# Optimization experiments

Measured on AMD Instinct MI355X. Metric: run time of the kernel, lower is better.

## Reference

```python
import jax, jax.numpy as jnp
import numpy as np

B, T, DIM, H = 2048, 16, 512, 8
INNER = 4 * DIM  # GEGLU inner dim
NUM_REL = 2 * T - 1


def _ln(x, g, b, eps=1e-5):
    m = jnp.mean(x, -1, keepdims=True)
    v = jnp.var(x, -1, keepdims=True)
    return (x - m) * jax.lax.rsqrt(v + eps) * g + b


def _temporal_attn(x, mask, g, b, wq, wk, wv, wo, bo, pe):
    # x: (B, T, C); mask: (1, T, T) bool; pe: (2T-1, C)
    Bn, Tn, C = x.shape
    d = C // H
    scale = d ** -0.5
    res = x
    xn = _ln(x, g, b)
    q = (xn @ wq).reshape(Bn, Tn, H, d).transpose(0, 2, 1, 3)  # (B,H,T,d)
    k = (xn @ wk).reshape(Bn, Tn, H, d).transpose(0, 2, 1, 3)
    v = (xn @ wv).reshape(Bn, Tn, H, d).transpose(0, 2, 1, 3)
    sim = jnp.einsum('bhmd,bhnd->bhmn', q, k)
    # contextual(2) relative position bias: project rel-pos embeddings through to_q/to_k
    rel = jnp.arange(Tn)[None, :] - jnp.arange(Tn)[:, None] + (Tn - 1)  # (T,T) in [0, 2T-2]
    P = pe[rel]                              # (T, T, C)
    Kr = (P @ wk).reshape(Tn, Tn, H, d)      # (T, T, H, d)
    Qr = (P @ wq).reshape(Tn, Tn, H, d)
    bias = jnp.einsum('bhmd,mnhd->bhmn', q, Kr) + jnp.einsum('bhnd,mnhd->bhmn', k, Qr)
    sim = (sim + bias) * scale
    sim = jnp.where(mask[:, None], sim, -jnp.finfo(sim.dtype).max)
    attn = jax.nn.softmax(sim, axis=-1)
    out = jnp.einsum('bhmn,bhnd->bhmd', attn, v)
    out = out.transpose(0, 2, 1, 3).reshape(Bn, Tn, C)
    return out @ wo + bo + res


def _geglu_ff(x, g, b, w1, b1, w2, b2):
    xn = _ln(x, g, b)
    h = xn @ w1 + b1                         # (B, T, 2*INNER)
    a, gate = jnp.split(h, 2, axis=-1)
    y = a * jax.nn.gelu(gate, approximate=False)
    return y @ w2 + b2 + x


def setup_inputs() -> dict:
    key = jax.random.key(0)
    ks = jax.random.split(key, 24)
    s = 0.02
    d = {
        'x': jax.random.normal(ks[0], (B, T, DIM), jnp.float32),
        'femb': jax.random.normal(ks[1], (T, DIM), jnp.float32),
        'attn_mask': jnp.ones((1, T, T), dtype=bool),
    }
    for i, base in [(2, '1'), (10, '2')]:
        d['n%s_g' % base] = jnp.ones((DIM,), jnp.float32)
        d['n%s_b' % base] = jnp.zeros((DIM,), jnp.float32)
        d['wq%s' % base] = jax.random.normal(ks[i], (DIM, DIM), jnp.float32) * s
        d['wk%s' % base] = jax.random.normal(ks[i + 1], (DIM, DIM), jnp.float32) * s
        d['wv%s' % base] = jax.random.normal(ks[i + 2], (DIM, DIM), jnp.float32) * s
        d['wo%s' % base] = jax.random.normal(ks[i + 3], (DIM, DIM), jnp.float32) * s
        d['bo%s' % base] = jnp.zeros((DIM,), jnp.float32)
        d['pe%s' % base] = jax.random.normal(ks[i + 4], (NUM_REL, DIM), jnp.float32) * s
    d['n3_g'] = jnp.ones((DIM,), jnp.float32)
    d['n3_b'] = jnp.zeros((DIM,), jnp.float32)
    d['ffw1'] = jax.random.normal(ks[20], (DIM, 2 * INNER), jnp.float32) * s
    d['ffb1'] = jnp.zeros((2 * INNER,), jnp.float32)
    d['ffw2'] = jax.random.normal(ks[21], (INNER, DIM), jnp.float32) * s
    d['ffb2'] = jnp.zeros((DIM,), jnp.float32)
    return d


def reference(x, femb,
              n1_g, n1_b, wq1, wk1, wv1, wo1, bo1, pe1,
              n2_g, n2_b, wq2, wk2, wv2, wo2, bo2, pe2,
              n3_g, n3_b, ffw1, ffb1, ffw2, ffb2,
              attn_mask):
    # femb is accepted but unused, matching TemporalTransformerBlock._forward
    x = _temporal_attn(x, attn_mask, n1_g, n1_b, wq1, wk1, wv1, wo1, bo1, pe1)
    x = _temporal_attn(x, attn_mask, n2_g, n2_b, wq2, wk2, wv2, wo2, bo2, pe2)
    x = _geglu_ff(x, n3_g, n3_b, ffw1, ffb1, ffw2, ffb2)
    return x
```

## Files before the change

### kernel.cpp

```cpp
#include <hip/hip_runtime.h>

typedef unsigned int uint;
typedef unsigned short ushort;

typedef float f32x4 __attribute__((ext_vector_type(4)));
typedef short bf16x8 __attribute__((ext_vector_type(8)));

using gas1 = const uint __attribute__((address_space(1)))*;
using las3 = uint __attribute__((address_space(3)))*;

static constexpr int TB    = 2048;
static constexpr int TT    = 16;
static constexpr int TD    = 512;
static constexpr int TH    = 8;
static constexpr int HD    = 64;
static constexpr int NROWS = TB * TT;
static constexpr int NREL  = 2 * TT - 1;
static constexpr int INNER = 2048;

__device__ __forceinline__ float bf2f(uint h) {
    union { uint u; float f; } x; x.u = h << 16; return x.f;
}
__device__ __forceinline__ ushort f2bf(float f) {
    union { float f; uint u; } x; x.f = f;
    uint r = x.u + 0x7fffu + ((x.u >> 16) & 1u);
    return (ushort)(r >> 16);
}
__device__ __forceinline__ void unpack8(uint4 v, float* f) {
    f[0] = bf2f(v.x & 0xffffu); f[1] = bf2f(v.x >> 16);
    f[2] = bf2f(v.y & 0xffffu); f[3] = bf2f(v.y >> 16);
    f[4] = bf2f(v.z & 0xffffu); f[5] = bf2f(v.z >> 16);
    f[6] = bf2f(v.w & 0xffffu); f[7] = bf2f(v.w >> 16);
}
__device__ __forceinline__ uint pck(float a, float b) {
    return (uint)f2bf(a) | ((uint)f2bf(b) << 16);
}
__device__ __forceinline__ uint4 pack8(const float* f) {
    return make_uint4(pck(f[0], f[1]), pck(f[2], f[3]), pck(f[4], f[5]), pck(f[6], f[7]));
}
__device__ __forceinline__ bool is_f32(const uint* probe) { return probe[0] == 0x3F800000u; }
__device__ __forceinline__ float ldraw(const void* p, size_t i, bool f32) {
    return f32 ? ((const float*)p)[i] : bf2f(((const ushort*)p)[i]);
}

struct TrP { const void* in[8]; ushort* out[8]; };
__global__ __launch_bounds__(256)
void tr8_k(TrP p, const uint* __restrict__ probe) {
    const bool f32 = is_f32(probe);
    const void* in  = p.in[blockIdx.z];
    ushort*     out = p.out[blockIdx.z];
    __shared__ ushort t[32][33];
    const int bx = blockIdx.x, by = blockIdx.y;
    const int x = threadIdx.x, y = threadIdx.y;
    #pragma unroll
    for (int i = 0; i < 4; ++i) {
        const size_t src = (size_t)(by * 32 + y + i * 8) * TD + bx * 32 + x;
        t[y + i * 8][x] = f32 ? f2bf(((const float*)in)[src]) : ((const ushort*)in)[src];
    }
    __syncthreads();
    #pragma unroll
    for (int i = 0; i < 4; ++i)
        out[(size_t)(bx * 32 + y + i * 8) * TD + by * 32 + x] = t[x][y + i * 8];
}

__global__ __launch_bounds__(256)
void transpose_k(const void* __restrict__ in, ushort* __restrict__ out, int R, int C,
                 const uint* __restrict__ probe) {
    const bool f32 = is_f32(probe);
    __shared__ ushort t[32][33];
    const int bx = blockIdx.x, by = blockIdx.y;
    const int x = threadIdx.x, y = threadIdx.y;
    #pragma unroll
    for (int i = 0; i < 4; ++i) {
        const size_t src = (size_t)(by * 32 + y + i * 8) * C + bx * 32 + x;
        t[y + i * 8][x] = f32 ? f2bf(((const float*)in)[src]) : ((const ushort*)in)[src];
    }
    __syncthreads();
    #pragma unroll
    for (int i = 0; i < 4; ++i)
        out[(size_t)(bx * 32 + y + i * 8) * R + by * 32 + x] = t[x][y + i * 8];
}

struct PewP { const void* pe[4]; const void* w[4]; ushort* out[4]; };
__global__ __launch_bounds__(256)
void pew4_k(PewP p, const uint* __restrict__ probe) {
    const bool f32 = is_f32(probe);
    const int z = blockIdx.z;
    const void* pe = p.pe[z];
    const void* w  = p.w[z];
    ushort*    out = p.out[z];
    const int c = blockIdx.x * 256 + threadIdx.x;
    const int r = blockIdx.y;
    float acc = 0.f;
    for (int k = 0; k < TD; ++k)
        acc += ldraw(pe, (size_t)r * TD + k, f32) * ldraw(w, (size_t)k * TD + c, f32);
    out[r * TD + c] = f2bf(acc);
}

template<bool RAW>
__global__ __launch_bounds__(256)
void ln_k(const void* __restrict__ xin, const void* __restrict__ gw,
          const void* __restrict__ bw, ushort* __restrict__ out,
          const uint* __restrict__ probe) {
    const bool f32 = is_f32(probe);
    const int row = blockIdx.x * 4 + (threadIdx.x >> 6);
    const int l = threadIdx.x & 63;
    const int c0 = l * 8;
    float v[8];
    if (RAW && f32) {
        const float* x = (const float*)xin + (size_t)row * TD + c0;
        const float4 a = *(const float4*)x;
        const float4 b = *(const float4*)(x + 4);
        v[0] = a.x; v[1] = a.y; v[2] = a.z; v[3] = a.w;
        v[4] = b.x; v[5] = b.y; v[6] = b.z; v[7] = b.w;
    } else {
        unpack8(*(const uint4*)((const ushort*)xin + (size_t)row * TD + c0), v);
    }
    float s = 0.f, s2 = 0.f;
    #pragma unroll
    for (int j = 0; j < 8; ++j) { s += v[j]; s2 += v[j] * v[j]; }
    #pragma unroll
    for (int off = 32; off; off >>= 1) {
        s  += __shfl_xor(s, off);
        s2 += __shfl_xor(s2, off);
    }
    const float mean = s * (1.f / TD);
    const float var  = s2 * (1.f / TD) - mean * mean;
    const float rstd = rsqrtf(var + 1e-5f);
    float gf[8], bf[8], r[8];
    if (f32) {
        const float* g = (const float*)gw + c0;
        const float* b = (const float*)bw + c0;
        #pragma unroll
        for (int j = 0; j < 8; ++j) { gf[j] = g[j]; bf[j] = b[j]; }
    } else {
        unpack8(*(const uint4*)((const ushort*)gw + c0), gf);
        unpack8(*(const uint4*)((const ushort*)bw + c0), bf);
    }
    #pragma unroll
    for (int j = 0; j < 8; ++j) r[j] = (v[j] - mean) * rstd * gf[j] + bf[j];
    *(uint4*)(out + (size_t)row * TD + c0) = pack8(r);
}

template<bool GEGLU>
__global__ __launch_bounds__(256)
void gemm_bt(const ushort* __restrict__ A, const ushort* __restrict__ Bt,
             const void* __restrict__ bias, const void* Res, void* C,
             int M, int N, int K, int resraw, int outraw, int outrow0,
             const uint* __restrict__ probe) {
    const bool f32 = is_f32(probe);
    constexpr int BN = GEGLU ? 64 : 128;
    constexpr int NI = GEGLU ? 2 : 4;
    __shared__ ushort sA[2][128 * 32];
    __shared__ ushort sB[2][BN * 32];
    __shared__ ushort sB2[GEGLU ? 2 : 1][GEGLU ? BN * 32 : 16];

    const int tid = threadIdx.x;

    const int lin = blockIdx.y * gridDim.x + blockIdx.x;
    const int cgx = gridDim.x >> 3;
    const int xcd = lin & 7;
    const int idx = lin >> 3;
    const int bx  = xcd * cgx + (idx % cgx);
    const int by  = idx / cgx;

    const int m0 = bx * 128;
    const int n0 = by * BN;
    const int w  = tid >> 6;
    const int l  = tid & 63;
    const int wm = (w >> 1) * 64;
    const int wn = (w & 1) * (BN / 2);
    const int fr = l & 15;
    const int fg = l >> 4;

    const int srow = tid >> 2;
    const int spart = (tid & 3) * 8;
    const ushort* gA0 = A  + (size_t)(m0 + srow) * K + spart;
    const ushort* gA1 = gA0 + (size_t)64 * K;
    const ushort* gB0 = Bt + (size_t)(n0 + srow) * K + spart;
    const ushort* gB1 = gB0 + (size_t)64 * K;
    const ushort* gG0 = Bt + (size_t)(N + n0 + srow) * K + spart;

    f32x4 acc[4][NI]  = {};
    f32x4 acc2[4][NI] = {};

    const int NT = K >> 5;

    auto stage = [&](int t, int buf) {
        const int kt = t * 32;
        __builtin_amdgcn_global_load_lds((gas1)(const void*)(gA0 + kt),
            (las3)(void*)(&sA[buf][tid * 8]), 16, 0, 0);
        __builtin_amdgcn_global_load_lds((gas1)(const void*)(gA1 + kt),
            (las3)(void*)(&sA[buf][(tid + 256) * 8]), 16, 0, 0);
        __builtin_amdgcn_global_load_lds((gas1)(const void*)(gB0 + kt),
            (las3)(void*)(&sB[buf][tid * 8]), 16, 0, 0);
        if constexpr (!GEGLU)
            __builtin_amdgcn_global_load_lds((gas1)(const void*)(gB1 + kt),
                (las3)(void*)(&sB[buf][(tid + 256) * 8]), 16, 0, 0);
        if constexpr (GEGLU)
            __builtin_amdgcn_global_load_lds((gas1)(const void*)(gG0 + kt),
                (las3)(void*)(&sB2[buf][tid * 8]), 16, 0, 0);
    };

    stage(0, 0);
    __syncthreads();

    for (int t = 0; t < NT; ++t) {
        const int cur = t & 1;
        if (t + 1 < NT) stage(t + 1, cur ^ 1);

        bf16x8 af[4], bn[NI], bg[NI];
        #pragma unroll
        for (int i = 0; i < 4; ++i)
            af[i] = *(const bf16x8*)&sA[cur][(wm + i * 16 + fr) * 32 + fg * 8];
        #pragma unroll
        for (int i = 0; i < NI; ++i) {
            bn[i] = *(const bf16x8*)&sB[cur][(wn + i * 16 + fr) * 32 + fg * 8];
            if constexpr (GEGLU)
                bg[i] = *(const bf16x8*)&sB2[cur][(wn + i * 16 + fr) * 32 + fg * 8];
        }
        #pragma unroll
        for (int mi = 0; mi < 4; ++mi)
            #pragma unroll
            for (int ni = 0; ni < NI; ++ni) {
                acc[mi][ni] = __builtin_amdgcn_mfma_f32_16x16x32_bf16(af[mi], bn[ni], acc[mi][ni], 0, 0, 0);
                if constexpr (GEGLU)
                    acc2[mi][ni] = __builtin_amdgcn_mfma_f32_16x16x32_bf16(af[mi], bg[ni], acc2[mi][ni], 0, 0, 0);
            }
        __syncthreads();
    }

    #pragma unroll
    for (int mi = 0; mi < 4; ++mi)
        #pragma unroll
        for (int ni = 0; ni < NI; ++ni) {
            const int col = n0 + wn + ni * 16 + fr;
            const float bv = bias ? ldraw(bias, col, f32) : 0.f;
            float bgv = 0.f;
            if constexpr (GEGLU) bgv = bias ? ldraw(bias, (size_t)N + col, f32) : 0.f;
            #pragma unroll
            for (int j = 0; j < 4; ++j) {
                const int row = m0 + wm + mi * 16 + fg * 4 + j;
                const size_t idx2 = (size_t)(outrow0 + row) * N + col;
                float v = acc[mi][ni][j] + bv;
                if constexpr (GEGLU) {
                    const float gt = acc2[mi][ni][j] + bgv;
                    v = v * (0.5f * gt * (1.f + erff(gt * 0.70710678118654752f)));
                }
                if (Res) v += resraw ? ldraw(Res, idx2, f32) : bf2f(((const ushort*)Res)[idx2]);
                if (outraw && f32) ((float*)C)[idx2] = v;
                else               ((ushort*)C)[idx2] = f2bf(v);
            }
        }
}

__global__ __launch_bounds__(64)
void attn_k(const ushort* __restrict__ qkv, const ushort* __restrict__ peWk,
            const ushort* __restrict__ peWq, ushort* __restrict__ out) {
    __shared__ ushort sQ[16][72], sK[16][72], sV[16][72];
    __shared__ ushort sPk[31][72], sPq[31][72];
    __shared__ float sP[16][20];

    const int tid = threadIdx.x;
    const int b = blockIdx.x >> 3;
    const int h = blockIdx.x & 7;
    const size_t rowbase = (size_t)b * 16 * (3 * TD) + h * HD;

    #pragma unroll
    for (int it = 0; it < 2; ++it) {
        const int c = tid + it * 64;
        const int m = c >> 3, part = c & 7;
        const ushort* src = qkv + rowbase + (size_t)m * (3 * TD) + part * 8;
        *(uint4*)&sQ[m][part * 8] = *(const uint4*)(src);
        *(uint4*)&sK[m][part * 8] = *(const uint4*)(src + TD);
        *(uint4*)&sV[m][part * 8] = *(const uint4*)(src + 2 * TD);
    }
    #pragma unroll
    for (int it = 0; it < 4; ++it) {
        const int c = tid + it * 64;
        if (c < NREL * 8) {
            const int r = c >> 3, part = c & 7;
            *(uint4*)&sPk[r][part * 8] = *(const uint4*)&peWk[(size_t)r * TD + h * HD + part * 8];
            *(uint4*)&sPq[r][part * 8] = *(const uint4*)&peWq[(size_t)r * TD + h * HD + part * 8];
        }
    }
    __syncthreads();

    const int m = tid & 15;
    const int g = tid >> 4;

    float aqk[4] = {0, 0, 0, 0}, ab1[4] = {0, 0, 0, 0}, ab2[4] = {0, 0, 0, 0};
    for (int dc = 0; dc < 8; ++dc) {
        float qf[8];
        unpack8(*(const uint4*)&sQ[m][dc * 8], qf);
        #pragma unroll
        for (int t = 0; t < 4; ++t) {
            const int n = g * 4 + t;
            const int rel = n - m + (TT - 1);
            float kf[8], pk[8], pq[8];
            unpack8(*(const uint4*)&sK[n][dc * 8], kf);
            unpack8(*(const uint4*)&sPk[rel][dc * 8], pk);
            unpack8(*(const uint4*)&sPq[rel][dc * 8], pq);
            #pragma unroll
            for (int j = 0; j < 8; ++j) {
                aqk[t] += qf[j] * kf[j];
                ab1[t] += qf[j] * pk[j];
                ab2[t] += kf[j] * pq[j];
            }
        }
    }
    float sim[4];
    #pragma unroll
    for (int t = 0; t < 4; ++t) sim[t] = (aqk[t] + ab1[t] + ab2[t]) * 0.125f;

    float mx = fmaxf(fmaxf(sim[0], sim[1]), fmaxf(sim[2], sim[3]));
    mx = fmaxf(mx, __shfl_xor(mx, 16));
    mx = fmaxf(mx, __shfl_xor(mx, 32));
    float e[4], ssum = 0.f;
    #pragma unroll
    for (int t = 0; t < 4; ++t) { e[t] = __expf(sim[t] - mx); ssum += e[t]; }
    ssum += __shfl_xor(ssum, 16);
    ssum += __shfl_xor(ssum, 32);
    const float inv = 1.f / ssum;
    #pragma unroll
    for (int t = 0; t < 4; ++t) sP[m][g * 4 + t] = e[t] * inv;
    __syncthreads();

    float o[16] = {};
    for (int n = 0; n < 16; ++n) {
        const float pv = sP[m][n];
        float vf[16];
        unpack8(*(const uint4*)&sV[n][g * 16], vf);
        unpack8(*(const uint4*)&sV[n][g * 16 + 8], vf + 8);
        #pragma unroll
        for (int i = 0; i < 16; ++i) o[i] += pv * vf[i];
    }
    ushort* dst = out + (size_t)(b * 16 + m) * TD + h * HD + g * 16;
    *(uint4*)dst = pack8(o);
    *(uint4*)(dst + 8) = pack8(o + 8);
}

extern "C" void kernel_launch(void* const* d_in, const int* in_sizes, int n_in,
                              void* d_out, int out_size, void* d_ws, size_t ws_size,
                              hipStream_t stream) {
    (void)in_sizes; (void)n_in; (void)out_size;

    const void* X   = d_in[0];
    const void* n1g = d_in[3];
    const void* n1b = d_in[4];
    const void* wq1 = d_in[5];
    const void* wk1 = d_in[6];
    const void* wv1 = d_in[7];
    const void* wo1 = d_in[8];
    const void* bo1 = d_in[9];
    const void* pe1 = d_in[10];
    const void* n2g = d_in[11];
    const void* n2b = d_in[12];
    const void* wq2 = d_in[13];
    const void* wk2 = d_in[14];
    const void* wv2 = d_in[15];
    const void* wo2 = d_in[16];
    const void* bo2 = d_in[17];
    const void* pe2 = d_in[18];
    const void* n3g = d_in[19];
    const void* n3b = d_in[20];
    const void* fw1 = d_in[21];
    const void* fb1 = d_in[22];
    const void* fw2 = d_in[23];
    const void* fb2 = d_in[24];
    const uint* probe = (const uint*)n1g;

    ushort* ws    = (ushort*)d_ws;
    ushort* xn    = ws;
    ushort* qkv   = xn + (size_t)NROWS * TD;
    ushort* x12   = qkv + (size_t)NROWS * (3 * TD);
    ushort* p     = x12 + (size_t)NROWS * TD;
    ushort* qkvT1 = p; p += (size_t)3 * TD * TD;
    ushort* woT1  = p; p += (size_t)TD * TD;
    ushort* qkvT2 = p; p += (size_t)3 * TD * TD;
    ushort* woT2  = p; p += (size_t)TD * TD;
    ushort* w1T   = p; p += (size_t)2 * INNER * TD;
    ushort* w2T   = p; p += (size_t)TD * INNER;
    ushort* peWk1 = p; p += NREL * TD;
    ushort* peWq1 = p; p += NREL * TD;
    ushort* peWk2 = p; p += NREL * TD;
    ushort* peWq2 = p; p += NREL * TD;
    const size_t need_bytes = (size_t)(p - ws) * sizeof(ushort);
    if (ws_size < need_bytes) return;

    ushort* aout = xn;
    ushort* ybuf = qkv;

    const dim3 tpb(32, 8);
    TrP trp;
    trp.in[0] = wq1; trp.out[0] = qkvT1;
    trp.in[1] = wk1; trp.out[1] = qkvT1 + TD * TD;
    trp.in[2] = wv1; trp.out[2] = qkvT1 + 2 * TD * TD;
    trp.in[3] = wo1; trp.out[3] = woT1;
    trp.in[4] = wq2; trp.out[4] = qkvT2;
    trp.in[5] = wk2; trp.out[5] = qkvT2 + TD * TD;
    trp.in[6] = wv2; trp.out[6] = qkvT2 + 2 * TD * TD;
    trp.in[7] = wo2; trp.out[7] = woT2;
    tr8_k<<<dim3(TD / 32, TD / 32, 8), tpb, 0, stream>>>(trp, probe);
    transpose_k<<<dim3(2 * INNER / 32, TD / 32), tpb, 0, stream>>>(fw1, w1T, TD, 2 * INNER, probe);
    transpose_k<<<dim3(TD / 32, INNER / 32), tpb, 0, stream>>>(fw2, w2T, INNER, TD, probe);
    PewP pwp;
    pwp.pe[0] = pe1; pwp.w[0] = wk1; pwp.out[0] = peWk1;
    pwp.pe[1] = pe1; pwp.w[1] = wq1; pwp.out[1] = peWq1;
    pwp.pe[2] = pe2; pwp.w[2] = wk2; pwp.out[2] = peWk2;
    pwp.pe[3] = pe2; pwp.w[3] = wq2; pwp.out[3] = peWq2;
    pew4_k<<<dim3(2, NREL, 4), 256, 0, stream>>>(pwp, probe);

    const int gm = NROWS / 128;

    ln_k<true><<<NROWS / 4, 256, 0, stream>>>(X, n1g, n1b, xn, probe);
    gemm_bt<false><<<dim3(gm, 12), 256, 0, stream>>>(
        xn, qkvT1, nullptr, nullptr, qkv, NROWS, 3 * TD, TD, 0, 0, 0, probe);
    attn_k<<<TB * TH, 64, 0, stream>>>(qkv, peWk1, peWq1, aout);
    gemm_bt<false><<<dim3(gm, 4), 256, 0, stream>>>(
        aout, woT1, bo1, X, x12, NROWS, TD, TD, 1, 0, 0, probe);

    ln_k<false><<<NROWS / 4, 256, 0, stream>>>(x12, n2g, n2b, xn, probe);
    gemm_bt<false><<<dim3(gm, 12), 256, 0, stream>>>(
        xn, qkvT2, nullptr, nullptr, qkv, NROWS, 3 * TD, TD, 0, 0, 0, probe);
    attn_k<<<TB * TH, 64, 0, stream>>>(qkv, peWk2, peWq2, aout);
    gemm_bt<false><<<dim3(gm, 4), 256, 0, stream>>>(
        aout, woT2, bo2, x12, x12, NROWS, TD, TD, 0, 0, 0, probe);

    ln_k<false><<<NROWS / 4, 256, 0, stream>>>(x12, n3g, n3b, xn, probe);
    const int chunk = NROWS / 2;
    for (int hh = 0; hh < 2; ++hh) {
        gemm_bt<true><<<dim3(chunk / 128, INNER / 64), 256, 0, stream>>>(
            xn + (size_t)hh * chunk * TD, w1T, fb1, nullptr, ybuf,
            chunk, INNER, TD, 0, 0, 0, probe);
        gemm_bt<false><<<dim3(chunk / 128, TD / 128), 256, 0, stream>>>(
            ybuf, w2T, fb2, (const void*)x12, d_out,
            chunk, TD, INNER, 0, 1, hh * chunk, probe);
    }
}
```

Before: 975.1 us.

## Triple-buffer GEMM LDS stages with partial vmcnt waits and XOR-swizzled layout

Moves the bf16 GEMM main loop from double to triple buffering so two k-tiles are in flight. Each iteration waits only until the oldest stage's loads have landed (s_waitcnt vmcnt) instead of a full __syncthreads. It also XOR-swizzles the 16-byte chunk position within each 32-element LDS row, on both the global source column and the fragment read offset, to cut bank conflicts on the MFMA fragment loads. This costs 50% more LDS per block, which may lower occupancy. The hardcoded vmcnt(4) assumes exactly four loads per stage, and the GEGLU variant issues four as well.

```diff
diff --git a/kernel.cpp b/kernel.cpp
--- a/kernel.cpp
+++ b/kernel.cpp
@@ -151,9 +151,9 @@
     const bool f32 = is_f32(probe);
     constexpr int BN = GEGLU ? 64 : 128;
     constexpr int NI = GEGLU ? 2 : 4;
-    __shared__ ushort sA[2][128 * 32];
-    __shared__ ushort sB[2][BN * 32];
-    __shared__ ushort sB2[GEGLU ? 2 : 1][GEGLU ? BN * 32 : 16];
+    __shared__ ushort sA[3][128 * 32];
+    __shared__ ushort sB[3][BN * 32];
+    __shared__ ushort sB2[GEGLU ? 3 : 1][GEGLU ? BN * 32 : 16];
 
     const int tid = threadIdx.x;
 
@@ -174,12 +174,12 @@
     const int fg = l >> 4;
 
     const int srow = tid >> 2;
-    const int spart = (tid & 3) * 8;
-    const ushort* gA0 = A  + (size_t)(m0 + srow) * K + spart;
+    const int gsp  = (((tid & 3) ^ ((srow >> 1) & 3))) * 8;
+    const ushort* gA0 = A  + (size_t)(m0 + srow) * K + gsp;
     const ushort* gA1 = gA0 + (size_t)64 * K;
-    const ushort* gB0 = Bt + (size_t)(n0 + srow) * K + spart;
+    const ushort* gB0 = Bt + (size_t)(n0 + srow) * K + gsp;
     const ushort* gB1 = gB0 + (size_t)64 * K;
-    const ushort* gG0 = Bt + (size_t)(N + n0 + srow) * K + spart;
+    const ushort* gG0 = Bt + (size_t)(N + n0 + srow) * K + gsp;
 
     f32x4 acc[4][NI]  = {};
     f32x4 acc2[4][NI] = {};
@@ -201,23 +201,27 @@
             __builtin_amdgcn_global_load_lds((gas1)(const void*)(gG0 + kt),
                 (las3)(void*)(&sB2[buf][tid * 8]), 16, 0, 0);
     };
+    auto lofs = [](int r, int g) { return (r * 4 + (g ^ ((r >> 1) & 3))) * 8; };
 
     stage(0, 0);
-    __syncthreads();
+    stage(1, 1);
+    asm volatile("s_waitcnt vmcnt(4)" ::: "memory");
+    __builtin_amdgcn_s_barrier();
 
     for (int t = 0; t < NT; ++t) {
-        const int cur = t & 1;
-        if (t + 1 < NT) stage(t + 1, cur ^ 1);
+        const int cur = t % 3;
+        if (t + 2 < NT) stage(t + 2, (t + 2) % 3);
+        __builtin_amdgcn_sched_barrier(0);
 
         bf16x8 af[4], bn[NI], bg[NI];
         #pragma unroll
         for (int i = 0; i < 4; ++i)
-            af[i] = *(const bf16x8*)&sA[cur][(wm + i * 16 + fr) * 32 + fg * 8];
+            af[i] = *(const bf16x8*)&sA[cur][lofs(wm + i * 16 + fr, fg)];
         #pragma unroll
         for (int i = 0; i < NI; ++i) {
-            bn[i] = *(const bf16x8*)&sB[cur][(wn + i * 16 + fr) * 32 + fg * 8];
+            bn[i] = *(const bf16x8*)&sB[cur][lofs(wn + i * 16 + fr, fg)];
             if constexpr (GEGLU)
-                bg[i] = *(const bf16x8*)&sB2[cur][(wn + i * 16 + fr) * 32 + fg * 8];
+                bg[i] = *(const bf16x8*)&sB2[cur][lofs(wn + i * 16 + fr, fg)];
         }
         #pragma unroll
         for (int mi = 0; mi < 4; ++mi)
@@ -227,7 +231,13 @@
                 if constexpr (GEGLU)
                     acc2[mi][ni] = __builtin_amdgcn_mfma_f32_16x16x32_bf16(af[mi], bg[ni], acc2[mi][ni], 0, 0, 0);
             }
-        __syncthreads();
+        __builtin_amdgcn_sched_barrier(0);
+        if (t + 2 < NT) {
+            asm volatile("s_waitcnt vmcnt(4)" ::: "memory");
+        } else {
+            asm volatile("s_waitcnt vmcnt(0)" ::: "memory");
+        }
+        __builtin_amdgcn_s_barrier();
     }
 
     #pragma unroll
```

After: 959.8 us. About the same (-1.6%).
